# Kernel tuning notes

Measured on AMD Instinct MI355X. Metric: run time of the kernel, lower is better.

## Reference

```python
import jax, jax.numpy as jnp
import numpy as np

B, C_IN, N, HC = 32, 128, 8192, 64
HEAD_NAMES = ['hm', 'reg', 'height', 'dim', 'rot', 'iou']
HEAD_OUT = [3, 2, 1, 3, 2, 1]
EPS = 1e-5
INIT_BIAS = -2.19


def setup_inputs() -> dict:
    key = jax.random.key(0)
    ks = jax.random.split(key, 16)
    d = {}
    d['ct_feat'] = jax.random.normal(ks[0], (B, C_IN, N), jnp.float32)
    # shared conv (1x1) + BN1d params
    d['sh_w'] = jax.random.normal(ks[1], (HC, C_IN), jnp.float32) * 0.05
    d['sh_b'] = jnp.zeros((HC,), jnp.float32)
    d['sh_g'] = jnp.ones((HC,), jnp.float32)
    d['sh_beta'] = jnp.zeros((HC,), jnp.float32)
    d['sh_mean'] = jax.random.normal(ks[2], (HC,), jnp.float32) * 0.1
    d['sh_var'] = jax.random.uniform(ks[3], (HC,), jnp.float32) + 0.5
    # first conv layer of each SepHead branch (stacked over 6 heads)
    d['head_w1'] = jax.random.normal(ks[4], (6, HC, HC), jnp.float32) * 0.05
    d['head_b1'] = jnp.zeros((6, HC), jnp.float32)
    d['head_g1'] = jnp.ones((6, HC), jnp.float32)
    d['head_beta1'] = jnp.zeros((6, HC), jnp.float32)
    d['head_mean1'] = jax.random.normal(ks[5], (6, HC), jnp.float32) * 0.1
    d['head_var1'] = jax.random.uniform(ks[6], (6, HC), jnp.float32) + 0.5
    # final conv of each branch (distinct out channels)
    for i, (name, c_out) in enumerate(zip(HEAD_NAMES, HEAD_OUT)):
        d[name + '_w'] = jax.random.normal(ks[7 + i], (c_out, HC), jnp.float32) * 0.05
        if name == 'hm':  # hm final bias is filled with init_bias
            d[name + '_b'] = jnp.full((c_out,), INIT_BIAS, jnp.float32)
        else:
            d[name + '_b'] = jnp.zeros((c_out,), jnp.float32)
    return d


def _bn(x, g, b, m, v):
    # x: [B, C, N]; params: [C]
    return (x - m[:, None]) * jax.lax.rsqrt(v[:, None] + EPS) * g[:, None] + b[:, None]


def reference(ct_feat, sh_w, sh_b, sh_g, sh_beta, sh_mean, sh_var,
              head_w1, head_b1, head_g1, head_beta1, head_mean1, head_var1,
              hm_w, hm_b, reg_w, reg_b, height_w, height_b,
              dim_w, dim_b, rot_w, rot_b, iou_w, iou_b):
    # shared_conv: Conv1d(k=1) + BN1d + ReLU
    y = jnp.einsum('oc,bcn->bon', sh_w, ct_feat) + sh_b[:, None]
    y = jax.nn.relu(_bn(y, sh_g, sh_beta, sh_mean, sh_var))  # [B, HC, N]

    # first layer of all 6 head branches, batched over head axis h
    z = jnp.einsum('hoc,bcn->hbon', head_w1, y) + head_b1[:, None, :, None]
    z = (z - head_mean1[:, None, :, None]) * jax.lax.rsqrt(head_var1[:, None, :, None] + EPS)
    z = z * head_g1[:, None, :, None] + head_beta1[:, None, :, None]
    z = jax.nn.relu(z)  # [6, B, HC, N]

    finals = [(hm_w, hm_b), (reg_w, reg_b), (height_w, height_b),
              (dim_w, dim_b), (rot_w, rot_b), (iou_w, iou_b)]
    outs = [jnp.einsum('oc,bcn->bon', w, z[i]) + b[:, None]
            for i, (w, b) in enumerate(finals)]
    # concat in head order [hm(3), reg(2), height(1), dim(3), rot(2), iou(1)] -> [B, 12, N]
    return jnp.concatenate(outs, axis=1)
```

## Files before the change

kernel.cpp:

```cpp
#include <hip/hip_runtime.h>
#include <hip/hip_bf16.h>
#include <cstdint>

typedef __attribute__((ext_vector_type(8))) short bf16x8;
typedef __attribute__((ext_vector_type(4))) float f32x4;

#define NCOL 8192
#define TILE 128

union FragU { uint32_t u[4]; bf16x8 v; uint4 q; };

__device__ __forceinline__ uint16_t f2bf(float f) {
  uint32_t x = __builtin_bit_cast(uint32_t, f);
  x += 0x7fffu + ((x >> 16) & 1u);
  return (uint16_t)(x >> 16);
}

__device__ __forceinline__ bf16x8 load_frag_f32(const float* __restrict__ p, float s) {
  const float4 a = *(const float4*)p;
  const float4 b = *(const float4*)(p + 4);
  FragU f;
  f.u[0] = (uint32_t)f2bf(a.x * s) | ((uint32_t)f2bf(a.y * s) << 16);
  f.u[1] = (uint32_t)f2bf(a.z * s) | ((uint32_t)f2bf(a.w * s) << 16);
  f.u[2] = (uint32_t)f2bf(b.x * s) | ((uint32_t)f2bf(b.y * s) << 16);
  f.u[3] = (uint32_t)f2bf(b.z * s) | ((uint32_t)f2bf(b.w * s) << 16);
  return f.v;
}

__global__ __launch_bounds__(256, 2) void centerhead_kernel(
    const float* __restrict__ ct,
    const float* __restrict__ shw,
    const float* __restrict__ shb, const float* __restrict__ shg,
    const float* __restrict__ shbeta, const float* __restrict__ shmean,
    const float* __restrict__ shvar,
    const float* __restrict__ w1,
    const float* __restrict__ b1, const float* __restrict__ g1,
    const float* __restrict__ beta1, const float* __restrict__ mean1,
    const float* __restrict__ var1,
    const float* __restrict__ hm_w, const float* __restrict__ hm_b,
    const float* __restrict__ reg_w, const float* __restrict__ reg_b,
    const float* __restrict__ height_w, const float* __restrict__ height_b,
    const float* __restrict__ dim_w, const float* __restrict__ dim_b,
    const float* __restrict__ rot_w, const float* __restrict__ rot_b,
    const float* __restrict__ iou_w, const float* __restrict__ iou_b,
    float* __restrict__ outp)
{
  __shared__ __align__(16) uint32_t sm_xz[9216];
  __shared__ __align__(16) uint32_t sm_y[4608];
  __shared__ __align__(16) float sm_ofsh[64];
  __shared__ __align__(16) float sm_ofh[384];
  __shared__ __align__(16) float sm_bias[16];

  const int t    = threadIdx.x;
  const int wv   = t >> 6;
  const int lane = t & 63;
  const int l15  = lane & 15;
  const int qd   = lane >> 4;
  const int bid  = blockIdx.x;
  const int b    = bid >> 6;
  const int col0 = (bid & 63) * TILE;
  const int nb   = wv * 32;

  if (t < 64) {
    float sc = shg[t] * rsqrtf(shvar[t] + 1e-5f);
    sm_ofsh[t] = (shb[t] - shmean[t]) * sc + shbeta[t];
  }
  for (int i = t; i < 384; i += 256) {
    float sc = g1[i] * rsqrtf(var1[i] + 1e-5f);
    sm_ofh[i] = (b1[i] - mean1[i]) * sc + beta1[i];
  }
  if (t < 16) {
    float v = 0.f;
    if (t < 3)       v = hm_b[t];
    else if (t < 5)  v = reg_b[t - 3];
    else if (t < 6)  v = height_b[t - 5];
    else if (t < 9)  v = dim_b[t - 6];
    else if (t < 11) v = rot_b[t - 9];
    else if (t < 12) v = iou_b[t - 11];
    sm_bias[t] = v;
  }

  {
    const int c2g = t >> 4;
    const int n0  = (t & 15) * 8;
    #pragma unroll
    for (int i = 0; i < 4; ++i) {
      const int c2 = i * 16 + c2g;
      const size_t base = ((size_t)(b * 128 + 2 * c2)) * NCOL + col0 + n0;
      const float4 ra0 = *(const float4*)(ct + base);
      const float4 ra1 = *(const float4*)(ct + base + 4);
      const float4 rb0 = *(const float4*)(ct + base + NCOL);
      const float4 rb1 = *(const float4*)(ct + base + NCOL + 4);
      uint32_t d0 = (uint32_t)f2bf(ra0.x) | ((uint32_t)f2bf(rb0.x) << 16);
      uint32_t d1 = (uint32_t)f2bf(ra0.y) | ((uint32_t)f2bf(rb0.y) << 16);
      uint32_t d2 = (uint32_t)f2bf(ra0.z) | ((uint32_t)f2bf(rb0.z) << 16);
      uint32_t d3 = (uint32_t)f2bf(ra0.w) | ((uint32_t)f2bf(rb0.w) << 16);
      uint32_t d4 = (uint32_t)f2bf(ra1.x) | ((uint32_t)f2bf(rb1.x) << 16);
      uint32_t d5 = (uint32_t)f2bf(ra1.y) | ((uint32_t)f2bf(rb1.y) << 16);
      uint32_t d6 = (uint32_t)f2bf(ra1.z) | ((uint32_t)f2bf(rb1.z) << 16);
      uint32_t d7 = (uint32_t)f2bf(ra1.w) | ((uint32_t)f2bf(rb1.w) << 16);
      uint32_t* dst = &sm_xz[c2 * 132 + n0];
      *(uint4*)(dst)     = make_uint4(d0, d1, d2, d3);
      *(uint4*)(dst + 4) = make_uint4(d4, d5, d6, d7);
    }
  }

  bf16x8 aw[4][4];
  #pragma unroll
  for (int mt = 0; mt < 4; ++mt) {
    const int row = mt * 16 + l15;
    const float sc = shg[row] * rsqrtf(shvar[row] + 1e-5f);
    #pragma unroll
    for (int kc = 0; kc < 4; ++kc)
      aw[mt][kc] = load_frag_f32(shw + row * 128 + kc * 32 + qd * 8, sc);
  }

  __syncthreads();

  f32x4 accY[4][2];
  #pragma unroll
  for (int mt = 0; mt < 4; ++mt)
    #pragma unroll
    for (int j = 0; j < 2; ++j)
      accY[mt][j] = (f32x4){0.f, 0.f, 0.f, 0.f};

  #pragma unroll
  for (int kc = 0; kc < 4; ++kc) {
    #pragma unroll
    for (int j = 0; j < 2; ++j) {
      FragU f;
      const int base = (kc * 16 + qd * 4) * 132 + nb + j * 16 + l15;
      f.u[0] = sm_xz[base];
      f.u[1] = sm_xz[base + 132];
      f.u[2] = sm_xz[base + 264];
      f.u[3] = sm_xz[base + 396];
      #pragma unroll
      for (int mt = 0; mt < 4; ++mt)
        accY[mt][j] = __builtin_amdgcn_mfma_f32_16x16x32_bf16(aw[mt][kc], f.v, accY[mt][j], 0, 0, 0);
    }
  }

  #pragma unroll
  for (int mt = 0; mt < 4; ++mt) {
    const int cb = mt * 16 + qd * 4;
    const f32x4 of = *(const f32x4*)&sm_ofsh[cb];
    #pragma unroll
    for (int j = 0; j < 2; ++j) {
      const f32x4 v = accY[mt][j];
      float y0 = fmaxf(v[0] + of[0], 0.f);
      float y1 = fmaxf(v[1] + of[1], 0.f);
      float y2 = fmaxf(v[2] + of[2], 0.f);
      float y3 = fmaxf(v[3] + of[3], 0.f);
      uint2 val;
      val.x = (uint32_t)f2bf(y0) | ((uint32_t)f2bf(y1) << 16);
      val.y = (uint32_t)f2bf(y2) | ((uint32_t)f2bf(y3) << 16);
      const int row = nb + j * 16 + l15;
      *(uint2*)&sm_y[row * 36 + mt * 8 + qd * 2] = val;
    }
  }

  const float* wf_ptr[6] = {hm_w, reg_w, height_w, dim_w, rot_w, iou_w};
  const int rowbase[6] = {0, 3, 5, 6, 9, 11};
  const int couts[6]   = {3, 2, 1, 3, 2, 1};

  bf16x8 a1[2][4][2];
  bf16x8 af[2][2];

  auto load_head = [&](int h, bf16x8 (&a1d)[4][2], bf16x8 (&afd)[2]) {
    #pragma unroll
    for (int mt = 0; mt < 4; ++mt) {
      const int row = mt * 16 + l15;
      const float sc = g1[h * 64 + row] * rsqrtf(var1[h * 64 + row] + 1e-5f);
      #pragma unroll
      for (int kc = 0; kc < 2; ++kc)
        a1d[mt][kc] = load_frag_f32(w1 + (h * 64 + row) * 64 + kc * 32 + qd * 8, sc);
    }
    const int rr = l15 - rowbase[h];
    const bool valid = (rr >= 0) && (rr < couts[h]);
    #pragma unroll
    for (int kc = 0; kc < 2; ++kc) {
      if (valid) {
        afd[kc] = load_frag_f32(wf_ptr[h] + rr * 64 + kc * 32 + qd * 8, 1.0f);
      } else {
        FragU f;
        f.q = make_uint4(0, 0, 0, 0);
        afd[kc] = f.v;
      }
    }
  };

  load_head(0, a1[0], af[0]);

  __syncthreads();

  f32x4 accO[2];
  accO[0] = (f32x4){0.f, 0.f, 0.f, 0.f};
  accO[1] = (f32x4){0.f, 0.f, 0.f, 0.f};

  #pragma unroll
  for (int h = 0; h < 6; ++h) {
    const int cur = h & 1;

    f32x4 accZ[4][2];
    #pragma unroll
    for (int mt = 0; mt < 4; ++mt)
      #pragma unroll
      for (int j = 0; j < 2; ++j)
        accZ[mt][j] = (f32x4){0.f, 0.f, 0.f, 0.f};

    #pragma unroll
    for (int kc = 0; kc < 2; ++kc) {
      #pragma unroll
      for (int j = 0; j < 2; ++j) {
        FragU f;
        f.q = *(const uint4*)&sm_y[(nb + j * 16 + l15) * 36 + kc * 16 + qd * 4];
        #pragma unroll
        for (int mt = 0; mt < 4; ++mt)
          accZ[mt][j] = __builtin_amdgcn_mfma_f32_16x16x32_bf16(a1[cur][mt][kc], f.v, accZ[mt][j], 0, 0, 0);
      }
    }

    if (h < 5) load_head(h + 1, a1[cur ^ 1], af[cur ^ 1]);

    uint32_t* zb = &sm_xz[cur * 4608];
    #pragma unroll
    for (int mt = 0; mt < 4; ++mt) {
      const int cb = h * 64 + mt * 16 + qd * 4;
      const f32x4 of = *(const f32x4*)&sm_ofh[cb];
      #pragma unroll
      for (int j = 0; j < 2; ++j) {
        const f32x4 v = accZ[mt][j];
        float z0 = fmaxf(v[0] + of[0], 0.f);
        float z1 = fmaxf(v[1] + of[1], 0.f);
        float z2 = fmaxf(v[2] + of[2], 0.f);
        float z3 = fmaxf(v[3] + of[3], 0.f);
        uint2 val;
        val.x = (uint32_t)f2bf(z0) | ((uint32_t)f2bf(z1) << 16);
        val.y = (uint32_t)f2bf(z2) | ((uint32_t)f2bf(z3) << 16);
        const int row = nb + j * 16 + l15;
        *(uint2*)&zb[row * 36 + mt * 8 + qd * 2] = val;
      }
    }

    #pragma unroll
    for (int kc = 0; kc < 2; ++kc) {
      #pragma unroll
      for (int j = 0; j < 2; ++j) {
        FragU f;
        f.q = *(const uint4*)&zb[(nb + j * 16 + l15) * 36 + kc * 16 + qd * 4];
        accO[j] = __builtin_amdgcn_mfma_f32_16x16x32_bf16(af[cur][kc], f.v, accO[j], 0, 0, 0);
      }
    }
  }

  if (qd < 3) {
    const f32x4 bs = *(const f32x4*)&sm_bias[qd * 4];
    #pragma unroll
    for (int j = 0; j < 2; ++j) {
      const int col = col0 + nb + j * 16 + l15;
      #pragma unroll
      for (int r = 0; r < 4; ++r) {
        const int row = qd * 4 + r;
        outp[((size_t)(b * 12 + row)) * NCOL + col] = accO[j][r] + bs[r];
      }
    }
  }
}

extern "C" void kernel_launch(void* const* d_in, const int* in_sizes, int n_in,
                              void* d_out, int out_size, void* d_ws, size_t ws_size,
                              hipStream_t stream) {
  (void)out_size; (void)d_ws; (void)ws_size;
  static const int sortedPos[25] = {
      0, 24, 19, 21, 20, 22, 23, 8, 3, 5, 4, 6, 7,
      12, 11, 16, 15, 10, 9, 2, 1, 18, 17, 14, 13};
  const bool sorted_order =
      (n_in == 25) && (in_sizes[1] == 3) && (in_sizes[2] == 192) &&
      (in_sizes[8] == 24576) && (in_sizes[24] == 8192);
  const float* p[25];
  for (int r = 0; r < 25; ++r)
    p[r] = (const float*)d_in[sorted_order ? sortedPos[r] : r];

  dim3 grid(2048), block(256);
  hipLaunchKernelGGL(centerhead_kernel, grid, block, 0, stream,
      p[0], p[1], p[2], p[3], p[4], p[5], p[6],
      p[7], p[8], p[9], p[10], p[11], p[12],
      p[13], p[14], p[15], p[16], p[17], p[18],
      p[19], p[20], p[21], p[22], p[23], p[24],
      (float*)d_out);
}
```

Measured before the change: 344.5 us.

## Precompute bf16 fragment-packed weights in a prep kernel and stream input directly

Adds a small prep kernel that folds BN scales into the weights, converts them to bf16 in MFMA fragment order, and writes them plus the bias offsets to the workspace. The main kernel then loads ready-made fragments from global memory (cache-resident) instead of converting weights per block. It also reads ct_feat straight from global into B fragments, dropping the LDS staging buffer. That cuts shared memory use and lets launch bounds rise to 4 blocks per CU. The trade-offs are an extra launch, strided uncoalesced-ish scalar global loads for the input, and repeated weight loads from L2.

```diff
diff --git a/kernel.cpp b/kernel.cpp
--- a/kernel.cpp
+++ b/kernel.cpp
@@ -6,7 +6,15 @@
 typedef __attribute__((ext_vector_type(4))) float f32x4;
 
 #define NCOL 8192
-#define TILE 128
+
+#define WS_AW 0
+#define WS_A1 8192
+#define WS_AF 32768
+#define WS_U16_TOTAL 38912
+#define WS_OFSH 19456
+#define WS_OFH  19520
+#define WS_BIAS 19904
+#define PREP_TOTAL (WS_U16_TOTAL + 464)
 
 union FragU { uint32_t u[4]; bf16x8 v; uint4 q; };
 
@@ -15,41 +23,86 @@
   x += 0x7fffu + ((x >> 16) & 1u);
   return (uint16_t)(x >> 16);
 }
-
-__device__ __forceinline__ bf16x8 load_frag_f32(const float* __restrict__ p, float s) {
-  const float4 a = *(const float4*)p;
-  const float4 b = *(const float4*)(p + 4);
-  FragU f;
-  f.u[0] = (uint32_t)f2bf(a.x * s) | ((uint32_t)f2bf(a.y * s) << 16);
-  f.u[1] = (uint32_t)f2bf(a.z * s) | ((uint32_t)f2bf(a.w * s) << 16);
-  f.u[2] = (uint32_t)f2bf(b.x * s) | ((uint32_t)f2bf(b.y * s) << 16);
-  f.u[3] = (uint32_t)f2bf(b.z * s) | ((uint32_t)f2bf(b.w * s) << 16);
-  return f.v;
-}
-
-__global__ __launch_bounds__(256, 2) void centerhead_kernel(
-    const float* __restrict__ ct,
-    const float* __restrict__ shw,
-    const float* __restrict__ shb, const float* __restrict__ shg,
-    const float* __restrict__ shbeta, const float* __restrict__ shmean,
-    const float* __restrict__ shvar,
-    const float* __restrict__ w1,
-    const float* __restrict__ b1, const float* __restrict__ g1,
-    const float* __restrict__ beta1, const float* __restrict__ mean1,
-    const float* __restrict__ var1,
+__device__ __forceinline__ uint32_t rne_bits(float f) {
+  uint32_t x = __builtin_bit_cast(uint32_t, f);
+  return x + 0x7fffu + ((x >> 16) & 1u);
+}
+__device__ __forceinline__ uint32_t pack_bf16(float lo, float hi) {
+  return __builtin_amdgcn_perm(rne_bits(hi), rne_bits(lo), 0x07060302u);
+}
+
+__global__ __launch_bounds__(256) void ch_prep(
+    const float* __restrict__ shw, const float* __restrict__ shb,
+    const float* __restrict__ shg, const float* __restrict__ shbeta,
+    const float* __restrict__ shmean, const float* __restrict__ shvar,
+    const float* __restrict__ w1, const float* __restrict__ b1,
+    const float* __restrict__ g1, const float* __restrict__ beta1,
+    const float* __restrict__ mean1, const float* __restrict__ var1,
     const float* __restrict__ hm_w, const float* __restrict__ hm_b,
     const float* __restrict__ reg_w, const float* __restrict__ reg_b,
     const float* __restrict__ height_w, const float* __restrict__ height_b,
     const float* __restrict__ dim_w, const float* __restrict__ dim_b,
     const float* __restrict__ rot_w, const float* __restrict__ rot_b,
     const float* __restrict__ iou_w, const float* __restrict__ iou_b,
+    uint16_t* __restrict__ wsq)
+{
+  const int e = blockIdx.x * 256 + threadIdx.x;
+  if (e >= PREP_TOTAL) return;
+  const int rowbase[6] = {0, 3, 5, 6, 9, 11};
+  const int couts[6]   = {3, 2, 1, 3, 2, 1};
+  const float* wfp[6]  = {hm_w, reg_w, height_w, dim_w, rot_w, iou_w};
+
+  if (e < WS_A1) {
+    const int i = e & 7, q = (e >> 3) & 3, kc = (e >> 5) & 3, m = e >> 7;
+    const int k = kc * 32 + q * 8 + i;
+    const float sc = shg[m] * rsqrtf(shvar[m] + 1e-5f);
+    wsq[e] = f2bf(shw[m * 128 + k] * sc);
+  } else if (e < WS_AF) {
+    const int e2 = e - WS_A1;
+    const int i = e2 & 7, q = (e2 >> 3) & 3, kc = (e2 >> 5) & 1,
+              m = (e2 >> 6) & 63, h = e2 >> 12;
+    const int k = kc * 32 + q * 8 + i, row = h * 64 + m;
+    const float sc = g1[row] * rsqrtf(var1[row] + 1e-5f);
+    wsq[e] = f2bf(w1[row * 64 + k] * sc);
+  } else if (e < WS_U16_TOTAL) {
+    const int e2 = e - WS_AF;
+    const int i = e2 & 7, q = (e2 >> 3) & 3, kc = (e2 >> 5) & 1,
+              m = (e2 >> 6) & 15, h = e2 >> 10;
+    const int k = kc * 32 + q * 8 + i, rr = m - rowbase[h];
+    const float v = (rr >= 0 && rr < couts[h]) ? wfp[h][rr * 64 + k] : 0.f;
+    wsq[e] = f2bf(v);
+  } else {
+    const int t2 = e - WS_U16_TOTAL;
+    float* wff = (float*)wsq;
+    float v = 0.f;
+    if (t2 < 64) {
+      const float sc = shg[t2] * rsqrtf(shvar[t2] + 1e-5f);
+      v = (shb[t2] - shmean[t2]) * sc + shbeta[t2];
+    } else if (t2 < 448) {
+      const int i = t2 - 64;
+      const float sc = g1[i] * rsqrtf(var1[i] + 1e-5f);
+      v = (b1[i] - mean1[i]) * sc + beta1[i];
+    } else {
+      const int i = t2 - 448;
+      if (i < 3)       v = hm_b[i];
+      else if (i < 5)  v = reg_b[i - 3];
+      else if (i < 6)  v = height_b[i - 5];
+      else if (i < 9)  v = dim_b[i - 6];
+      else if (i < 11) v = rot_b[i - 9];
+      else if (i < 12) v = iou_b[i - 11];
+    }
+    wff[WS_OFSH + t2] = v;
+  }
+}
+
+__global__ __launch_bounds__(256, 4) void ch_main(
+    const float* __restrict__ ct,
+    const uint16_t* __restrict__ wsq,
+    const float* __restrict__ wsf,
     float* __restrict__ outp)
 {
-  __shared__ __align__(16) uint32_t sm_xz[9216];
   __shared__ __align__(16) uint32_t sm_y[4608];
-  __shared__ __align__(16) float sm_ofsh[64];
-  __shared__ __align__(16) float sm_ofh[384];
-  __shared__ __align__(16) float sm_bias[16];
+  __shared__ __align__(16) uint32_t sm_z[4608];
 
   const int t    = threadIdx.x;
   const int wv   = t >> 6;
@@ -58,64 +111,11 @@
   const int qd   = lane >> 4;
   const int bid  = blockIdx.x;
   const int b    = bid >> 6;
-  const int col0 = (bid & 63) * TILE;
+  const int col0 = (bid & 63) * 128;
   const int nb   = wv * 32;
 
-  if (t < 64) {
-    float sc = shg[t] * rsqrtf(shvar[t] + 1e-5f);
-    sm_ofsh[t] = (shb[t] - shmean[t]) * sc + shbeta[t];
-  }
-  for (int i = t; i < 384; i += 256) {
-    float sc = g1[i] * rsqrtf(var1[i] + 1e-5f);
-    sm_ofh[i] = (b1[i] - mean1[i]) * sc + beta1[i];
-  }
-  if (t < 16) {
-    float v = 0.f;
-    if (t < 3)       v = hm_b[t];
-    else if (t < 5)  v = reg_b[t - 3];
-    else if (t < 6)  v = height_b[t - 5];
-    else if (t < 9)  v = dim_b[t - 6];
-    else if (t < 11) v = rot_b[t - 9];
-    else if (t < 12) v = iou_b[t - 11];
-    sm_bias[t] = v;
-  }
-
-  {
-    const int c2g = t >> 4;
-    const int n0  = (t & 15) * 8;
-    #pragma unroll
-    for (int i = 0; i < 4; ++i) {
-      const int c2 = i * 16 + c2g;
-      const size_t base = ((size_t)(b * 128 + 2 * c2)) * NCOL + col0 + n0;
-      const float4 ra0 = *(const float4*)(ct + base);
-      const float4 ra1 = *(const float4*)(ct + base + 4);
-      const float4 rb0 = *(const float4*)(ct + base + NCOL);
-      const float4 rb1 = *(const float4*)(ct + base + NCOL + 4);
-      uint32_t d0 = (uint32_t)f2bf(ra0.x) | ((uint32_t)f2bf(rb0.x) << 16);
-      uint32_t d1 = (uint32_t)f2bf(ra0.y) | ((uint32_t)f2bf(rb0.y) << 16);
-      uint32_t d2 = (uint32_t)f2bf(ra0.z) | ((uint32_t)f2bf(rb0.z) << 16);
-      uint32_t d3 = (uint32_t)f2bf(ra0.w) | ((uint32_t)f2bf(rb0.w) << 16);
-      uint32_t d4 = (uint32_t)f2bf(ra1.x) | ((uint32_t)f2bf(rb1.x) << 16);
-      uint32_t d5 = (uint32_t)f2bf(ra1.y) | ((uint32_t)f2bf(rb1.y) << 16);
-      uint32_t d6 = (uint32_t)f2bf(ra1.z) | ((uint32_t)f2bf(rb1.z) << 16);
-      uint32_t d7 = (uint32_t)f2bf(ra1.w) | ((uint32_t)f2bf(rb1.w) << 16);
-      uint32_t* dst = &sm_xz[c2 * 132 + n0];
-      *(uint4*)(dst)     = make_uint4(d0, d1, d2, d3);
-      *(uint4*)(dst + 4) = make_uint4(d4, d5, d6, d7);
-    }
-  }
-
-  bf16x8 aw[4][4];
-  #pragma unroll
-  for (int mt = 0; mt < 4; ++mt) {
-    const int row = mt * 16 + l15;
-    const float sc = shg[row] * rsqrtf(shvar[row] + 1e-5f);
-    #pragma unroll
-    for (int kc = 0; kc < 4; ++kc)
-      aw[mt][kc] = load_frag_f32(shw + row * 128 + kc * 32 + qd * 8, sc);
-  }
-
-  __syncthreads();
+  const float* ctb = ct + (size_t)b * 128 * NCOL;
+  const int voff0 = qd * 8 * NCOL + col0 + nb + l15;
 
   f32x4 accY[4][2];
   #pragma unroll
@@ -126,72 +126,43 @@
 
   #pragma unroll
   for (int kc = 0; kc < 4; ++kc) {
+    bf16x8 a[4];
+    #pragma unroll
+    for (int mt = 0; mt < 4; ++mt) {
+      FragU fa;
+      fa.q = *(const uint4*)(wsq + WS_AW + ((mt * 16 + l15) * 4 + kc) * 32 + qd * 8);
+      a[mt] = fa.v;
+    }
     #pragma unroll
     for (int j = 0; j < 2; ++j) {
       FragU f;
-      const int base = (kc * 16 + qd * 4) * 132 + nb + j * 16 + l15;
-      f.u[0] = sm_xz[base];
-      f.u[1] = sm_xz[base + 132];
-      f.u[2] = sm_xz[base + 264];
-      f.u[3] = sm_xz[base + 396];
+      #pragma unroll
+      for (int i2 = 0; i2 < 4; ++i2) {
+        const size_t off = (size_t)((kc * 32 + 2 * i2) * NCOL) + voff0 + j * 16;
+        f.u[i2] = pack_bf16(ctb[off], ctb[off + NCOL]);
+      }
       #pragma unroll
       for (int mt = 0; mt < 4; ++mt)
-        accY[mt][j] = __builtin_amdgcn_mfma_f32_16x16x32_bf16(aw[mt][kc], f.v, accY[mt][j], 0, 0, 0);
+        accY[mt][j] = __builtin_amdgcn_mfma_f32_16x16x32_bf16(a[mt], f.v, accY[mt][j], 0, 0, 0);
     }
   }
 
   #pragma unroll
   for (int mt = 0; mt < 4; ++mt) {
-    const int cb = mt * 16 + qd * 4;
-    const f32x4 of = *(const f32x4*)&sm_ofsh[cb];
+    const f32x4 of = *(const f32x4*)(wsf + WS_OFSH + mt * 16 + qd * 4);
     #pragma unroll
     for (int j = 0; j < 2; ++j) {
       const f32x4 v = accY[mt][j];
-      float y0 = fmaxf(v[0] + of[0], 0.f);
-      float y1 = fmaxf(v[1] + of[1], 0.f);
-      float y2 = fmaxf(v[2] + of[2], 0.f);
-      float y3 = fmaxf(v[3] + of[3], 0.f);
+      const float y0 = fmaxf(v[0] + of[0], 0.f);
+      const float y1 = fmaxf(v[1] + of[1], 0.f);
+      const float y2 = fmaxf(v[2] + of[2], 0.f);
+      const float y3 = fmaxf(v[3] + of[3], 0.f);
       uint2 val;
-      val.x = (uint32_t)f2bf(y0) | ((uint32_t)f2bf(y1) << 16);
-      val.y = (uint32_t)f2bf(y2) | ((uint32_t)f2bf(y3) << 16);
-      const int row = nb + j * 16 + l15;
-      *(uint2*)&sm_y[row * 36 + mt * 8 + qd * 2] = val;
-    }
-  }
-
-  const float* wf_ptr[6] = {hm_w, reg_w, height_w, dim_w, rot_w, iou_w};
-  const int rowbase[6] = {0, 3, 5, 6, 9, 11};
-  const int couts[6]   = {3, 2, 1, 3, 2, 1};
-
-  bf16x8 a1[2][4][2];
-  bf16x8 af[2][2];
-
-  auto load_head = [&](int h, bf16x8 (&a1d)[4][2], bf16x8 (&afd)[2]) {
-    #pragma unroll
-    for (int mt = 0; mt < 4; ++mt) {
-      const int row = mt * 16 + l15;
-      const float sc = g1[h * 64 + row] * rsqrtf(var1[h * 64 + row] + 1e-5f);
-      #pragma unroll
-      for (int kc = 0; kc < 2; ++kc)
-        a1d[mt][kc] = load_frag_f32(w1 + (h * 64 + row) * 64 + kc * 32 + qd * 8, sc);
-    }
-    const int rr = l15 - rowbase[h];
-    const bool valid = (rr >= 0) && (rr < couts[h]);
-    #pragma unroll
-    for (int kc = 0; kc < 2; ++kc) {
-      if (valid) {
-        afd[kc] = load_frag_f32(wf_ptr[h] + rr * 64 + kc * 32 + qd * 8, 1.0f);
-      } else {
-        FragU f;
-        f.q = make_uint4(0, 0, 0, 0);
-        afd[kc] = f.v;
-      }
-    }
-  };
-
-  load_head(0, a1[0], af[0]);
-
-  __syncthreads();
+      val.x = pack_bf16(y0, y1);
+      val.y = pack_bf16(y2, y3);
+      *(uint2*)&sm_y[(nb + j * 16 + l15) * 36 + mt * 8 + qd * 2] = val;
+    }
+  }
 
   f32x4 accO[2];
   accO[0] = (f32x4){0.f, 0.f, 0.f, 0.f};
@@ -199,8 +170,6 @@
 
   #pragma unroll
   for (int h = 0; h < 6; ++h) {
-    const int cur = h & 1;
-
     f32x4 accZ[4][2];
     #pragma unroll
     for (int mt = 0; mt < 4; ++mt)
@@ -210,59 +179,61 @@
 
     #pragma unroll
     for (int kc = 0; kc < 2; ++kc) {
+      bf16x8 a[4];
+      #pragma unroll
+      for (int mt = 0; mt < 4; ++mt) {
+        FragU fa;
+        fa.q = *(const uint4*)(wsq + WS_A1 + ((h * 64 + mt * 16 + l15) * 2 + kc) * 32 + qd * 8);
+        a[mt] = fa.v;
+      }
       #pragma unroll
       for (int j = 0; j < 2; ++j) {
         FragU f;
         f.q = *(const uint4*)&sm_y[(nb + j * 16 + l15) * 36 + kc * 16 + qd * 4];
         #pragma unroll
         for (int mt = 0; mt < 4; ++mt)
-          accZ[mt][j] = __builtin_amdgcn_mfma_f32_16x16x32_bf16(a1[cur][mt][kc], f.v, accZ[mt][j], 0, 0, 0);
-      }
-    }
-
-    if (h < 5) load_head(h + 1, a1[cur ^ 1], af[cur ^ 1]);
-
-    uint32_t* zb = &sm_xz[cur * 4608];
+          accZ[mt][j] = __builtin_amdgcn_mfma_f32_16x16x32_bf16(a[mt], f.v, accZ[mt][j], 0, 0, 0);
+      }
+    }
+
     #pragma unroll
     for (int mt = 0; mt < 4; ++mt) {
-      const int cb = h * 64 + mt * 16 + qd * 4;
-      const f32x4 of = *(const f32x4*)&sm_ofh[cb];
+      const f32x4 of = *(const f32x4*)(wsf + WS_OFH + h * 64 + mt * 16 + qd * 4);
       #pragma unroll
       for (int j = 0; j < 2; ++j) {
         const f32x4 v = accZ[mt][j];
-        float z0 = fmaxf(v[0] + of[0], 0.f);
-        float z1 = fmaxf(v[1] + of[1], 0.f);
-        float z2 = fmaxf(v[2] + of[2], 0.f);
-        float z3 = fmaxf(v[3] + of[3], 0.f);
+        const float z0 = fmaxf(v[0] + of[0], 0.f);
+        const float z1 = fmaxf(v[1] + of[1], 0.f);
+        const float z2 = fmaxf(v[2] + of[2], 0.f);
+        const float z3 = fmaxf(v[3] + of[3], 0.f);
         uint2 val;
-        val.x = (uint32_t)f2bf(z0) | ((uint32_t)f2bf(z1) << 16);
-        val.y = (uint32_t)f2bf(z2) | ((uint32_t)f2bf(z3) << 16);
-        const int row = nb + j * 16 + l15;
-        *(uint2*)&zb[row * 36 + mt * 8 + qd * 2] = val;
+        val.x = pack_bf16(z0, z1);
+        val.y = pack_bf16(z2, z3);
+        *(uint2*)&sm_z[(nb + j * 16 + l15) * 36 + mt * 8 + qd * 2] = val;
       }
     }
 
     #pragma unroll
     for (int kc = 0; kc < 2; ++kc) {
+      FragU fa;
+      fa.q = *(const uint4*)(wsq + WS_AF + ((h * 16 + l15) * 2 + kc) * 32 + qd * 8);
       #pragma unroll
       for (int j = 0; j < 2; ++j) {
         FragU f;
-        f.q = *(const uint4*)&zb[(nb + j * 16 + l15) * 36 + kc * 16 + qd * 4];
-        accO[j] = __builtin_amdgcn_mfma_f32_16x16x32_bf16(af[cur][kc], f.v, accO[j], 0, 0, 0);
+        f.q = *(const uint4*)&sm_z[(nb + j * 16 + l15) * 36 + kc * 16 + qd * 4];
+        accO[j] = __builtin_amdgcn_mfma_f32_16x16x32_bf16(fa.v, f.v, accO[j], 0, 0, 0);
       }
     }
   }
 
   if (qd < 3) {
-    const f32x4 bs = *(const f32x4*)&sm_bias[qd * 4];
+    const f32x4 bs = *(const f32x4*)(wsf + WS_BIAS + qd * 4);
     #pragma unroll
     for (int j = 0; j < 2; ++j) {
       const int col = col0 + nb + j * 16 + l15;
       #pragma unroll
-      for (int r = 0; r < 4; ++r) {
-        const int row = qd * 4 + r;
-        outp[((size_t)(b * 12 + row)) * NCOL + col] = accO[j][r] + bs[r];
-      }
+      for (int r = 0; r < 4; ++r)
+        outp[((size_t)(b * 12 + qd * 4 + r)) * NCOL + col] = accO[j][r] + bs[r];
     }
   }
 }
@@ -270,7 +241,7 @@
 extern "C" void kernel_launch(void* const* d_in, const int* in_sizes, int n_in,
                               void* d_out, int out_size, void* d_ws, size_t ws_size,
                               hipStream_t stream) {
-  (void)out_size; (void)d_ws; (void)ws_size;
+  (void)out_size; (void)ws_size;
   static const int sortedPos[25] = {
       0, 24, 19, 21, 20, 22, 23, 8, 3, 5, 4, 6, 7,
       12, 11, 16, 15, 10, 9, 2, 1, 18, 17, 14, 13};
@@ -281,11 +252,15 @@
   for (int r = 0; r < 25; ++r)
     p[r] = (const float*)d_in[sorted_order ? sortedPos[r] : r];
 
-  dim3 grid(2048), block(256);
-  hipLaunchKernelGGL(centerhead_kernel, grid, block, 0, stream,
-      p[0], p[1], p[2], p[3], p[4], p[5], p[6],
+  uint16_t* wsq = (uint16_t*)d_ws;
+
+  hipLaunchKernelGGL(ch_prep, dim3((PREP_TOTAL + 255) / 256), dim3(256), 0, stream,
+      p[1], p[2], p[3], p[4], p[5], p[6],
       p[7], p[8], p[9], p[10], p[11], p[12],
       p[13], p[14], p[15], p[16], p[17], p[18],
       p[19], p[20], p[21], p[22], p[23], p[24],
-      (float*)d_out);
-}
+      wsq);
+
+  hipLaunchKernelGGL(ch_main, dim3(2048), dim3(256), 0, stream,
+      p[0], (const uint16_t*)wsq, (const float*)wsq, (float*)d_out);
+}
```

After: 294.7 us. 14.5% less time.
